# Optimization experiments

Hardware: AMD Instinct MI355X
Metric: run time of the kernel (lower is better)

## Reference

```python
import jax, jax.numpy as jnp
import numpy as np


def setup_inputs() -> dict:
    key = jax.random.key(0)
    ks = jax.random.split(key, 10)
    B, D_X, D_H, D_S, D_T = 16384, 256, 512, 128, 128
    G = 4 * D_H
    sc = lambda d: 1.0 / np.sqrt(d)
    return {
        "x": jax.random.normal(ks[0], (B, D_X), jnp.float32),
        "h": jax.random.normal(ks[1], (B, D_H), jnp.float32),
        "c": jax.random.normal(ks[2], (B, D_H), jnp.float32),
        "spatial_per_step": jax.random.normal(ks[3], (B, D_S), jnp.float32),
        "temporal_per_step": jax.random.normal(ks[4], (B, D_T), jnp.float32),
        "W_x": jax.random.normal(ks[5], (D_X, G), jnp.float32) * sc(D_X),
        "W_h": jax.random.normal(ks[6], (D_H, G), jnp.float32) * sc(D_H),
        "b_h": jax.random.normal(ks[7], (G,), jnp.float32) * 0.01,
        "W_s": jax.random.normal(ks[8], (D_S, G), jnp.float32) * sc(D_S),
        "W_t": jax.random.normal(ks[9], (D_T, G), jnp.float32) * sc(D_T),
    }


def reference(x, h, c, spatial_per_step, temporal_per_step, W_x, W_h, b_h, W_s, W_t):
    H = W_h.shape[0]  # hidden_size
    # Four gate projections summed (the fusion opportunity): [B, 4H]
    preact = (x @ W_x) + (h @ W_h + b_h) + (spatial_per_step @ W_s) + (temporal_per_step @ W_t)
    i_g = jax.nn.sigmoid(preact[:, 0 * H:1 * H])
    f_g = jax.nn.sigmoid(preact[:, 1 * H:2 * H])
    o_g = jax.nn.sigmoid(preact[:, 2 * H:3 * H])
    c_g = jnp.tanh(preact[:, 3 * H:4 * H])
    c_new = f_g * c + i_g * c_g
    # NOTE: faithful to the source, h = tanh(o * c) (not o * tanh(c))
    h_new = jnp.tanh(o_g * c_new)
    return (h_new, c_new)
```

## Files before the change

kernel.cpp:

```cpp
#include <hip/hip_runtime.h>
#include <hip/hip_bf16.h>
#include <cstdint>

#define B_DIM 16384
#define DX 256
#define DH 512
#define DS 128
#define DT 128
#define KDIM 1024
#define NDIM 2048
#define HOUT 512

#define NT 32
#define PAN 8192

typedef __attribute__((ext_vector_type(8))) short short8;
typedef __attribute__((ext_vector_type(4))) float floatx4;

union bf16x8 {
  short8 v;
  __hip_bfloat16 b[8];
};

__device__ __forceinline__ float fast_sigmoid(float x) {
  return 1.f / (1.f + __expf(-x));
}
__device__ __forceinline__ float fast_tanh(float x) {
  float e = __expf(-2.f * x);
  return (1.f - e) / (1.f + e);
}


__global__ __launch_bounds__(256) void pack_AW(
    const float* __restrict__ x, const float* __restrict__ h,
    const float* __restrict__ sp_, const float* __restrict__ tp_,
    const float* __restrict__ Wx, const float* __restrict__ Wh,
    const float* __restrict__ Ws, const float* __restrict__ Wt,
    __hip_bfloat16* __restrict__ Ap, __hip_bfloat16* __restrict__ Wp) {
  const int NA = B_DIM * KDIM / 8 / 256;
  const int bid = blockIdx.x;
  if (bid < NA) {
    int tid = bid * 256 + threadIdx.x;
    int i = tid & 63;
    int t32 = (tid >> 6) & 31;
    int tile = tid >> 11;
    int kb = tile & 15, mb = tile >> 4;
    int s = t32 >> 4, c = t32 & 15;
    int row = c * 16 + (i >> 2);
    int kq = (i & 3) ^ ((row >> 1) & 3);
    int b = mb * 256 + row;
    int k = kb * 64 + s * 32 + kq * 8;
    const float* p;
    if (k < 768) {
      p = (k < 256) ? (x + (size_t)b * DX + k) : (h + (size_t)b * DH + (k - 256));
    } else {
      p = (k < 896) ? (sp_ + (size_t)b * DS + (k - 768))
                    : (tp_ + (size_t)b * DT + (k - 896));
    }
    floatx4 v0 = *(const floatx4*)p;
    floatx4 v1 = *(const floatx4*)(p + 4);
    bf16x8 o;
#pragma unroll
    for (int j = 0; j < 4; ++j) {
      o.b[j]     = __float2bfloat16(v0[j]);
      o.b[4 + j] = __float2bfloat16(v1[j]);
    }
    *(short8*)(Ap + (size_t)tid * 8) = o.v;
  } else {
    int tid = (bid - NA) * 256 + threadIdx.x;
    int i = tid & 63;
    int t32 = (tid >> 6) & 31;
    int tile = tid >> 11;
    int kb = tile & 15, nb = tile >> 4;
    int s = t32 >> 4, c = t32 & 15;
    int pcol = c * 16 + (i >> 2);
    int kq = (i & 3) ^ ((pcol >> 1) & 3);
    int k = kb * 64 + s * 32 + kq * 8;
    int wn = pcol >> 6, g = (pcol >> 4) & 3, hl = pcol & 15;
    int col = g * 512 + nb * 64 + wn * 16 + hl;
    const float* src; int kl;
    if (k < 256)      { src = Wx; kl = k; }
    else if (k < 768) { src = Wh; kl = k - 256; }
    else if (k < 896) { src = Ws; kl = k - 768; }
    else              { src = Wt; kl = k - 896; }
    bf16x8 o;
#pragma unroll
    for (int r = 0; r < 8; ++r)
      o.b[r] = __float2bfloat16(src[(size_t)(kl + r) * NDIM + col]);
    *(short8*)(Wp + (size_t)tid * 8) = o.v;
  }
}

#define GLD(src, dst)                                              \
  __builtin_amdgcn_global_load_lds(                                \
      (const __attribute__((address_space(1))) void*)(src),        \
      (__attribute__((address_space(3))) void*)(dst), 16, 0, 0)

__global__ __launch_bounds__(512, 2) void lstm_gemm(
    const __hip_bfloat16* __restrict__ Ap, const __hip_bfloat16* __restrict__ Wp,
    const float* __restrict__ bh, const float* __restrict__ c_in,
    float* __restrict__ out) {
  extern __shared__ unsigned short smem[];
  unsigned short* As = smem;
  unsigned short* Bs = smem + 3 * PAN;

  const int tid = threadIdx.x;
  const int lane = tid & 63;
  const int wid = tid >> 6;
  const int wm = wid & 1;
  const int wn = wid >> 1;
  const int q = lane >> 4;
  const int fr = lane & 15;

  const int bid = blockIdx.x;
  const int wg = (bid & 7) * 64 + (bid >> 3);
  const int mb = wg >> 3;
  const int nb = wg & 7;
  const int m0 = mb * 256;

  int aOff[8], bOff[4];
#pragma unroll
  for (int m = 0; m < 8; ++m) {
    int row = wm * 128 + m * 16 + fr;
    aOff[m] = row * 32 + (q ^ ((row >> 1) & 3)) * 8;
  }
#pragma unroll
  for (int n = 0; n < 4; ++n) {
    int prow = wn * 64 + n * 16 + fr;
    bOff[n] = prow * 32 + (q ^ ((prow >> 1) & 3)) * 8;
  }

  floatx4 acc[8][4];
#pragma unroll
  for (int i = 0; i < 8; ++i)
#pragma unroll
    for (int j = 0; j < 4; ++j) acc[i][j] = (floatx4)0.f;

  const int ch0 = wid * 2;
  const __hip_bfloat16* aStg = Ap + (size_t)mb * 262144 + ch0 * 512 + lane * 8;
  const __hip_bfloat16* bStg = Wp + (size_t)nb * 262144 + ch0 * 512 + lane * 8;
  const int dA = ch0 * 512;

  GLD(aStg,              &As[dA]);        GLD(aStg + 512,        &As[dA + 512]);
  GLD(bStg,              &Bs[dA]);        GLD(bStg + 512,        &Bs[dA + 512]);
  GLD(aStg + 8192,       &As[PAN + dA]);  GLD(aStg + 8192 + 512, &As[PAN + dA + 512]);
  GLD(bStg + 8192,       &Bs[PAN + dA]);  GLD(bStg + 8192 + 512, &Bs[PAN + dA + 512]);
  asm volatile("s_waitcnt vmcnt(4)\n\ts_barrier" ::: "memory");

  int sR = 0;
  int sS = 2;

  for (int t = 0; t < NT; ++t) {
    const unsigned short* Ar = As + sR * PAN;
    const unsigned short* Br = Bs + sR * PAN;
    const int ts = (t + 2 < NT) ? (t + 2) : (NT - 1);
    const __hip_bfloat16* aP = aStg + (size_t)ts * PAN;
    const __hip_bfloat16* bP = bStg + (size_t)ts * PAN;
    unsigned short* Aw = As + sS * PAN;
    unsigned short* Bw = Bs + sS * PAN;

    GLD(aP, &Aw[dA]);
    GLD(aP + 512, &Aw[dA + 512]);
    short8 a0[4], bf[4];
#pragma unroll
    for (int i = 0; i < 4; ++i) a0[i] = *(const short8*)(Ar + aOff[i]);
#pragma unroll
    for (int i = 0; i < 4; ++i) bf[i] = *(const short8*)(Br + bOff[i]);
    asm volatile("s_barrier" ::: "memory");
    __builtin_amdgcn_sched_barrier(0);
    __builtin_amdgcn_s_setprio(1);
#pragma unroll
    for (int mi = 0; mi < 4; ++mi)
#pragma unroll
      for (int ni = 0; ni < 4; ++ni)
        acc[mi][ni] = __builtin_amdgcn_mfma_f32_16x16x32_bf16(
            a0[mi], bf[ni], acc[mi][ni], 0, 0, 0);
    __builtin_amdgcn_s_setprio(0);

    GLD(bP, &Bw[dA]);
    GLD(bP + 512, &Bw[dA + 512]);
    short8 a1[4];
#pragma unroll
    for (int i = 0; i < 4; ++i) a1[i] = *(const short8*)(Ar + aOff[4 + i]);
    asm volatile("s_waitcnt vmcnt(4)\n\ts_barrier" ::: "memory");
    __builtin_amdgcn_sched_barrier(0);
    __builtin_amdgcn_s_setprio(1);
#pragma unroll
    for (int mi = 0; mi < 4; ++mi)
#pragma unroll
      for (int ni = 0; ni < 4; ++ni)
        acc[4 + mi][ni] = __builtin_amdgcn_mfma_f32_16x16x32_bf16(
            a1[mi], bf[ni], acc[4 + mi][ni], 0, 0, 0);
    __builtin_amdgcn_s_setprio(0);

    sR = (sR == 2) ? 0 : sR + 1;
    sS = (sS == 2) ? 0 : sS + 1;
  }

  const int hh = nb * 64 + wn * 16 + fr;
  float bias[4];
#pragma unroll
  for (int g = 0; g < 4; ++g) bias[g] = bh[g * 512 + hh];

#pragma unroll
  for (int mi = 0; mi < 8; ++mi) {
#pragma unroll
    for (int r = 0; r < 4; ++r) {
      const size_t grow = (size_t)(m0 + wm * 128 + mi * 16 + q * 4 + r);
      const float pi = acc[mi][0][r] + bias[0];
      const float pf = acc[mi][1][r] + bias[1];
      const float po = acc[mi][2][r] + bias[2];
      const float pc = acc[mi][3][r] + bias[3];
      const float ig = fast_sigmoid(pi);
      const float fg = fast_sigmoid(pf);
      const float og = fast_sigmoid(po);
      const float cg = fast_tanh(pc);
      const float cc = fg * c_in[grow * HOUT + hh] + ig * cg;
      out[grow * HOUT + hh] = fast_tanh(og * cc);
      out[(size_t)B_DIM * HOUT + grow * HOUT + hh] = cc;
    }
  }
}

extern "C" void kernel_launch(void* const* d_in, const int* in_sizes, int n_in,
                              void* d_out, int out_size, void* d_ws, size_t ws_size,
                              hipStream_t stream) {
  const float* x  = (const float*)d_in[0];
  const float* h  = (const float*)d_in[1];
  const float* c  = (const float*)d_in[2];
  const float* sp = (const float*)d_in[3];
  const float* tp = (const float*)d_in[4];
  const float* Wx = (const float*)d_in[5];
  const float* Wh = (const float*)d_in[6];
  const float* bh = (const float*)d_in[7];
  const float* Ws = (const float*)d_in[8];
  const float* Wt = (const float*)d_in[9];
  float* out = (float*)d_out;

  __hip_bfloat16* Ap = (__hip_bfloat16*)d_ws;
  __hip_bfloat16* Wp = (__hip_bfloat16*)((char*)d_ws + (size_t)B_DIM * KDIM * 2);

  static bool attr_done = false;
  if (!attr_done) {
    hipFuncSetAttribute((const void*)lstm_gemm,
                        hipFuncAttributeMaxDynamicSharedMemorySize, 98304);
    attr_done = true;
  }

  const int nblk_A = B_DIM * KDIM / 8 / 256;
  const int nblk_W = NDIM * KDIM / 8 / 256;
  pack_AW<<<dim3(nblk_A + nblk_W), dim3(256), 0, stream>>>(
      x, h, sp, tp, Wx, Wh, Ws, Wt, Ap, Wp);
  lstm_gemm<<<dim3(512), dim3(512), 98304, stream>>>(Ap, Wp, bh, c, out);
}
```

Measured before the change: 232.9 us.

## Halve GEMM block N-tile to 128 with 4-wave blocks and 1024 workgroups

Shrinks each GEMM workgroup from a 256x256 output tile with 8 waves to a 256x128 tile with 4 waves. The weight-packing layout, the LDS panel sizes, the staging loads and the wait counts change to match, and the grid doubles to 1024 blocks. The aim is more, smaller workgroups with less LDS each, to improve scheduling and latency hiding. The cost is that activation panels are re-read by twice as many column blocks, which doubles A-side global and L2 traffic and lowers reuse per loaded byte.

```diff
diff --git a/kernel.cpp b/kernel.cpp
--- a/kernel.cpp
+++ b/kernel.cpp
@@ -12,7 +12,8 @@
 #define HOUT 512
 
 #define NT 32
-#define PAN 8192
+#define APAN 8192
+#define BPAN 4096
 
 typedef __attribute__((ext_vector_type(8))) short short8;
 typedef __attribute__((ext_vector_type(4))) float floatx4;
@@ -69,15 +70,15 @@
   } else {
     int tid = (bid - NA) * 256 + threadIdx.x;
     int i = tid & 63;
-    int t32 = (tid >> 6) & 31;
-    int tile = tid >> 11;
-    int kb = tile & 15, nb = tile >> 4;
-    int s = t32 >> 4, c = t32 & 15;
+    int t16 = (tid >> 6) & 15;
+    int tile = tid >> 10;
+    int kb = tile & 15, nblk = tile >> 4;
+    int s = t16 >> 3, c = t16 & 7;
     int pcol = c * 16 + (i >> 2);
     int kq = (i & 3) ^ ((pcol >> 1) & 3);
     int k = kb * 64 + s * 32 + kq * 8;
     int wn = pcol >> 6, g = (pcol >> 4) & 3, hl = pcol & 15;
-    int col = g * 512 + nb * 64 + wn * 16 + hl;
+    int col = g * 512 + nblk * 32 + wn * 16 + hl;
     const float* src; int kl;
     if (k < 256)      { src = Wx; kl = k; }
     else if (k < 768) { src = Wh; kl = k - 256; }
@@ -96,13 +97,13 @@
       (const __attribute__((address_space(1))) void*)(src),        \
       (__attribute__((address_space(3))) void*)(dst), 16, 0, 0)
 
-__global__ __launch_bounds__(512, 2) void lstm_gemm(
+__global__ __launch_bounds__(256, 2) void lstm_gemm(
     const __hip_bfloat16* __restrict__ Ap, const __hip_bfloat16* __restrict__ Wp,
     const float* __restrict__ bh, const float* __restrict__ c_in,
     float* __restrict__ out) {
   extern __shared__ unsigned short smem[];
   unsigned short* As = smem;
-  unsigned short* Bs = smem + 3 * PAN;
+  unsigned short* Bs = smem + 3 * APAN;
 
   const int tid = threadIdx.x;
   const int lane = tid & 63;
@@ -113,9 +114,9 @@
   const int fr = lane & 15;
 
   const int bid = blockIdx.x;
-  const int wg = (bid & 7) * 64 + (bid >> 3);
-  const int mb = wg >> 3;
-  const int nb = wg & 7;
+  const int wg = (bid & 7) * 128 + (bid >> 3);
+  const int mb = wg >> 4;
+  const int nblk = wg & 15;
   const int m0 = mb * 256;
 
   int aOff[8], bOff[4];
@@ -126,8 +127,8 @@
   }
 #pragma unroll
   for (int n = 0; n < 4; ++n) {
-    int prow = wn * 64 + n * 16 + fr;
-    bOff[n] = prow * 32 + (q ^ ((prow >> 1) & 3)) * 8;
+    int pc = wn * 64 + n * 16 + fr;
+    bOff[n] = pc * 32 + (q ^ ((pc >> 1) & 3)) * 8;
   }
 
   floatx4 acc[8][4];
@@ -136,31 +137,36 @@
 #pragma unroll
     for (int j = 0; j < 4; ++j) acc[i][j] = (floatx4)0.f;
 
-  const int ch0 = wid * 2;
-  const __hip_bfloat16* aStg = Ap + (size_t)mb * 262144 + ch0 * 512 + lane * 8;
-  const __hip_bfloat16* bStg = Wp + (size_t)nb * 262144 + ch0 * 512 + lane * 8;
-  const int dA = ch0 * 512;
-
-  GLD(aStg,              &As[dA]);        GLD(aStg + 512,        &As[dA + 512]);
-  GLD(bStg,              &Bs[dA]);        GLD(bStg + 512,        &Bs[dA + 512]);
-  GLD(aStg + 8192,       &As[PAN + dA]);  GLD(aStg + 8192 + 512, &As[PAN + dA + 512]);
-  GLD(bStg + 8192,       &Bs[PAN + dA]);  GLD(bStg + 8192 + 512, &Bs[PAN + dA + 512]);
-  asm volatile("s_waitcnt vmcnt(4)\n\ts_barrier" ::: "memory");
+  const int ca = wid * 4, cb = wid * 2;
+  const __hip_bfloat16* aStg = Ap + (size_t)mb * 262144 + ca * 512 + lane * 8;
+  const __hip_bfloat16* bStg = Wp + (size_t)nblk * 131072 + cb * 512 + lane * 8;
+  const int dA = ca * 512, dB = cb * 512;
+
+#pragma unroll
+  for (int T = 0; T < 2; ++T) {
+#pragma unroll
+    for (int j = 0; j < 4; ++j)
+      GLD(aStg + (size_t)T * APAN + j * 512, &As[T * APAN + dA + j * 512]);
+#pragma unroll
+    for (int j = 0; j < 2; ++j)
+      GLD(bStg + (size_t)T * BPAN + j * 512, &Bs[T * BPAN + dB + j * 512]);
+  }
+  asm volatile("s_waitcnt vmcnt(6)\n\ts_barrier" ::: "memory");
 
   int sR = 0;
   int sS = 2;
 
   for (int t = 0; t < NT; ++t) {
-    const unsigned short* Ar = As + sR * PAN;
-    const unsigned short* Br = Bs + sR * PAN;
+    const unsigned short* Ar = As + sR * APAN;
+    const unsigned short* Br = Bs + sR * BPAN;
     const int ts = (t + 2 < NT) ? (t + 2) : (NT - 1);
-    const __hip_bfloat16* aP = aStg + (size_t)ts * PAN;
-    const __hip_bfloat16* bP = bStg + (size_t)ts * PAN;
-    unsigned short* Aw = As + sS * PAN;
-    unsigned short* Bw = Bs + sS * PAN;
-
-    GLD(aP, &Aw[dA]);
-    GLD(aP + 512, &Aw[dA + 512]);
+    const __hip_bfloat16* aP = aStg + (size_t)ts * APAN;
+    const __hip_bfloat16* bP = bStg + (size_t)ts * BPAN;
+    unsigned short* Aw = As + sS * APAN;
+    unsigned short* Bw = Bs + sS * BPAN;
+
+#pragma unroll
+    for (int j = 0; j < 4; ++j) GLD(aP + j * 512, &Aw[dA + j * 512]);
     short8 a0[4], bf[4];
 #pragma unroll
     for (int i = 0; i < 4; ++i) a0[i] = *(const short8*)(Ar + aOff[i]);
@@ -177,12 +183,12 @@
             a0[mi], bf[ni], acc[mi][ni], 0, 0, 0);
     __builtin_amdgcn_s_setprio(0);
 
-    GLD(bP, &Bw[dA]);
-    GLD(bP + 512, &Bw[dA + 512]);
+#pragma unroll
+    for (int j = 0; j < 2; ++j) GLD(bP + j * 512, &Bw[dB + j * 512]);
     short8 a1[4];
 #pragma unroll
     for (int i = 0; i < 4; ++i) a1[i] = *(const short8*)(Ar + aOff[4 + i]);
-    asm volatile("s_waitcnt vmcnt(4)\n\ts_barrier" ::: "memory");
+    asm volatile("s_waitcnt vmcnt(6)\n\ts_barrier" ::: "memory");
     __builtin_amdgcn_sched_barrier(0);
     __builtin_amdgcn_s_setprio(1);
 #pragma unroll
@@ -197,7 +203,7 @@
     sS = (sS == 2) ? 0 : sS + 1;
   }
 
-  const int hh = nb * 64 + wn * 16 + fr;
+  const int hh = nblk * 32 + wn * 16 + fr;
   float bias[4];
 #pragma unroll
   for (int g = 0; g < 4; ++g) bias[g] = bh[g * 512 + hh];
@@ -243,7 +249,7 @@
   static bool attr_done = false;
   if (!attr_done) {
     hipFuncSetAttribute((const void*)lstm_gemm,
-                        hipFuncAttributeMaxDynamicSharedMemorySize, 98304);
+                        hipFuncAttributeMaxDynamicSharedMemorySize, 73728);
     attr_done = true;
   }
 
@@ -251,5 +257,5 @@
   const int nblk_W = NDIM * KDIM / 8 / 256;
   pack_AW<<<dim3(nblk_A + nblk_W), dim3(256), 0, stream>>>(
       x, h, sp, tp, Wx, Wh, Ws, Wt, Ap, Wp);
-  lstm_gemm<<<dim3(512), dim3(512), 98304, stream>>>(Ap, Wp, bh, c, out);
-}
+  lstm_gemm<<<dim3(1024), dim3(256), 73728, stream>>>(Ap, Wp, bh, c, out);
+}
```

Result: no change. 237.3 us (+1.9%).
